# Kernel tuning notes

Hardware: AMD Instinct MI355X
Metric: run time of the kernel (lower is better)

## Reference

```python
import jax, jax.numpy as jnp
import numpy as np

B, S, D, H = 4, 2048, 1024, 16
HD = D // H


def setup_inputs() -> dict:
    key = jax.random.key(0)
    ks = jax.random.split(key, 10)
    x = jax.random.normal(ks[0], (B, S, D), dtype=jnp.float32)
    mask = jnp.zeros((B, 1, 1, S), dtype=jnp.float32)  # 1 = masked, 0 = keep
    sc = 1.0 / np.sqrt(D)
    wq = jax.random.normal(ks[1], (D, D), dtype=jnp.float32) * sc
    wk = jax.random.normal(ks[2], (D, D), dtype=jnp.float32) * sc
    wv = jax.random.normal(ks[3], (D, D), dtype=jnp.float32) * sc
    wo = jax.random.normal(ks[4], (D, D), dtype=jnp.float32) * sc
    bq = jnp.zeros((D,), jnp.float32)
    bk = jnp.zeros((D,), jnp.float32)
    bv = jnp.zeros((D,), jnp.float32)
    bo = jnp.zeros((D,), jnp.float32)
    return {"x": x, "mask": mask, "wq": wq, "bq": bq, "wk": wk, "bk": bk,
            "wv": wv, "bv": bv, "wo": wo, "bo": bo}


def _split_heads(t):
    # (B, S, D) -> (B, H, S, HD)
    return t.reshape(B, -1, H, HD).transpose(0, 2, 1, 3)


def reference(x, mask, wq, bq, wk, bk, wv, bv, wo, bo):
    q = _split_heads(x @ wq + bq)
    k = _split_heads(x @ wk + bk)
    v = _split_heads(x @ wv + bv)
    # scaled dot-product attention (TF tutorial convention: mask*-1e9 added)
    scores = jnp.einsum("bhqd,bhkd->bhqk", q, k) / jnp.sqrt(jnp.float32(HD))
    scores = scores + mask * -1e9
    attn_weights = jax.nn.softmax(scores, axis=-1)  # (B, H, Sq, Sk)
    attn = jnp.einsum("bhqk,bhkd->bhqd", attn_weights, v)
    attn = attn.transpose(0, 2, 1, 3).reshape(B, -1, D)
    out = attn @ wo + bo
    return out, attn_weights
```

## Files before the change

### kernel.cpp

```cpp
#include <hip/hip_runtime.h>
#include <hip/hip_bf16.h>

#define S_LEN  2048
#define DMODEL 1024
#define NHEAD  16
#define HDIM   64
#define BSZ    4

#define C_SCORE  0.18033688f
#define C_MASK  -1.4426950e9f

typedef __bf16 bf16_t;
typedef __bf16 bf16x8 __attribute__((ext_vector_type(8)));
typedef __bf16 bf16x4 __attribute__((ext_vector_type(4)));
typedef float  f32x4  __attribute__((ext_vector_type(4)));

typedef __attribute__((address_space(1))) void as1_void;
typedef __attribute__((address_space(3))) void as3_void;

__device__ __forceinline__ f32x4 mfma16(bf16x8 a, bf16x8 b, f32x4 c) {
    return __builtin_amdgcn_mfma_f32_16x16x32_bf16(a, b, c, 0, 0, 0);
}

__global__ __launch_bounds__(256) void cvt_all(const float* __restrict__ x,
                                               bf16_t* __restrict__ xb,
                                               const float* __restrict__ w0,
                                               const float* __restrict__ w1,
                                               const float* __restrict__ w2,
                                               const float* __restrict__ w3,
                                               bf16_t* __restrict__ wT) {
    __shared__ bf16_t t[64][65];
    const int bid = blockIdx.x;
    if (bid < 4096) {
        const int i0 = bid * 256 + threadIdx.x;
        #pragma unroll
        for (int rep = 0; rep < 2; ++rep) {
            const int i = i0 + rep * 1048576;
            float4 v = ((const float4*)x)[i];
            bf16x4 tv = { (bf16_t)v.x, (bf16_t)v.y, (bf16_t)v.z, (bf16_t)v.w };
            ((bf16x4*)xb)[i] = tv;
        }
        return;
    }
    const int wb = bid - 4096;
    const int wsel = wb >> 8;
    const float* w = wsel == 0 ? w0 : (wsel == 1 ? w1 : (wsel == 2 ? w2 : w3));
    bf16_t* wTo = wT + (size_t)wsel * DMODEL * DMODEL;
    const int rb = wb & 255;
    const int bx = (rb & 15) * 64, by = (rb >> 4) * 64;
    const int tx = threadIdx.x & 63, ty = threadIdx.x >> 6;
    #pragma unroll
    for (int rr = 0; rr < 64; rr += 4)
        t[tx][rr + ty] = (bf16_t)w[(size_t)(bx + rr + ty) * DMODEL + by + tx];
    __syncthreads();
    #pragma unroll
    for (int rr = 0; rr < 64; rr += 4)
        wTo[(size_t)(by + rr + ty) * DMODEL + bx + tx] = t[rr + ty][tx];
}

template <int MODE>
__global__ __launch_bounds__(256) void gemm_bt(const bf16_t* __restrict__ A,
                                               const bf16_t* __restrict__ Bt,
                                               const float* __restrict__ b0,
                                               const float* __restrict__ b1,
                                               const float* __restrict__ b2,
                                               bf16_t* __restrict__ o0,
                                               bf16_t* __restrict__ o1,
                                               bf16_t* __restrict__ o2,
                                               float* __restrict__ of) {
    constexpr int GK = 1024;
    __shared__ __attribute__((aligned(16))) bf16_t smem_ab[8704];
    bf16_t* As = smem_ab;
    bf16_t* Bs = smem_ab + 4096;

    const int tid  = threadIdx.x;
    const int wave = tid >> 6, lane = tid & 63;
    const int col16 = lane & 15, g = lane >> 4;
    const int wr = wave >> 1, wc = wave & 1;
    const int bn0 = blockIdx.x * 128, bm0 = blockIdx.y * 128;

    const int r4 = tid >> 2;
    const int c8 = (tid & 3) * 8;

    f32x4 acc[4][4] = {};

    for (int k0 = 0; k0 < GK; k0 += 32) {
        __syncthreads();
        #pragma unroll
        for (int i = 0; i < 2; ++i) {
            __builtin_amdgcn_global_load_lds(
                (const as1_void*)(A + (size_t)(bm0 + i * 64 + r4) * GK + k0 + c8),
                (as3_void*)(As + (i * 64 + wave * 16) * 32), 16, 0, 0);
            __builtin_amdgcn_global_load_lds(
                (const as1_void*)(Bt + (size_t)(bn0 + i * 64 + r4) * GK + k0 + c8),
                (as3_void*)(Bs + (i * 64 + wave * 16) * 32), 16, 0, 0);
        }
        __syncthreads();

        bf16x8 af[4], bfr[4];
        #pragma unroll
        for (int i = 0; i < 4; ++i) {
            af[i]  = *(const bf16x8*)(As + (wr * 64 + i * 16 + col16) * 32 + g * 8);
            bfr[i] = *(const bf16x8*)(Bs + (wc * 64 + i * 16 + col16) * 32 + g * 8);
        }
        #pragma unroll
        for (int mi = 0; mi < 4; ++mi)
            #pragma unroll
            for (int ni = 0; ni < 4; ++ni)
                acc[mi][ni] = mfma16(af[mi], bfr[ni], acc[mi][ni]);
    }

    if (MODE == 0 && (bn0 >> 10) == 2) {
        const int n1base = bn0 - 2048;
        const int brow = bm0 >> 11;
        const int s0 = bm0 & 2047;
        __syncthreads();
        #pragma unroll
        for (int p = 0; p < 2; ++p) {
            if (p) __syncthreads();
            if (wc == p) {
                #pragma unroll
                for (int ni = 0; ni < 4; ++ni) {
                    const float bv = b2[n1base + p * 64 + ni * 16 + col16];
                    #pragma unroll
                    for (int mi = 0; mi < 4; ++mi) {
                        bf16x4 pv;
                        #pragma unroll
                        for (int r = 0; r < 4; ++r) pv[r] = (bf16_t)(acc[mi][ni][r] + bv);
                        *(bf16x4*)&smem_ab[(ni * 16 + col16) * 136 + wr * 64 + mi * 16 + g * 4] = pv;
                    }
                }
            }
            __syncthreads();
            const int h2 = (n1base + p * 64) >> 6;
            bf16_t* vout = o2 + (((size_t)brow * NHEAD + h2) * HDIM) * S_LEN + s0;
            #pragma unroll
            for (int j = 0; j < 4; ++j) {
                const int unit = j * 256 + tid;
                const int row = unit >> 4;
                const int cu = (unit & 15) * 8;
                bf16x8 v = *(const bf16x8*)&smem_ab[row * 136 + cu];
                *(bf16x8*)(vout + (size_t)row * S_LEN + cu) = v;
            }
        }
        return;
    }

    #pragma unroll
    for (int ni = 0; ni < 4; ++ni) {
        const int gn = bn0 + wc * 64 + ni * 16 + col16;
        if (MODE == 0) {
            const int proj = bn0 >> 10;
            const float* bias = proj == 0 ? b0 : b1;
            bf16_t* outp      = proj == 0 ? o0 : o1;
            const int n1 = gn & 1023, h = n1 >> 6, hd = n1 & 63;
            const float bv = bias[n1];
            #pragma unroll
            for (int mi = 0; mi < 4; ++mi)
                #pragma unroll
                for (int r = 0; r < 4; ++r) {
                    const int gm = bm0 + wr * 64 + mi * 16 + g * 4 + r;
                    const int b = gm >> 11, s = gm & 2047;
                    outp[(((size_t)b * NHEAD + h) * S_LEN + s) * HDIM + hd] =
                        (bf16_t)(acc[mi][ni][r] + bv);
                }
        } else {
            const float bv = b0[gn];
            #pragma unroll
            for (int mi = 0; mi < 4; ++mi)
                #pragma unroll
                for (int r = 0; r < 4; ++r) {
                    const int gm = bm0 + wr * 64 + mi * 16 + g * 4 + r;
                    of[(size_t)gm * DMODEL + gn] = acc[mi][ni][r] + bv;
                }
        }
    }
}

__global__ __launch_bounds__(256, 2) void attn_fused(const bf16_t* __restrict__ Q,
                                                     const bf16_t* __restrict__ K,
                                                     const bf16_t* __restrict__ Vt,
                                                     const float* __restrict__ mask,
                                                     float* __restrict__ attnW,
                                                     bf16_t* __restrict__ ctx) {
    __shared__ __attribute__((aligned(16))) char smem[73728];
    bf16_t (*KsA)[128][64] = (bf16_t(*)[128][64])smem;
    bf16_t (*Ks)[64][64]   = (bf16_t(*)[64][64])smem;
    bf16_t (*Vs)[64][64]   = (bf16_t(*)[64][64])(smem + 16384);
    float  (*Pl)[32][64]   = (float(*)[32][64])(smem + 32768);
    float*  Ml             = (float*)(smem + 65536);

    const int tid = threadIdx.x, wave = tid >> 6, lane = tid & 63;
    const int col16 = lane & 15, g = lane >> 4;
    const int r7 = col16 & 7;

    const int lin = blockIdx.x;
    const int logical = (lin & 7) * 64 + (lin >> 3);
    const int bh = logical >> 3, pp = logical & 7;
    const int b = bh >> 4, h = bh & 15;
    const int qA = pp * 256 + wave * 32;
    const int qB = pp * 256 + 128 + wave * 32;

    const bf16_t* Qb = Q + (size_t)bh * S_LEN * HDIM;
    const bf16_t* Kb = K + (size_t)bh * S_LEN * HDIM;
    const bf16_t* Vb = Vt + (size_t)bh * HDIM * S_LEN;
    const float* mp = mask + (size_t)b * S_LEN;

    #pragma unroll
    for (int i = 0; i < 2; ++i) {
        const int idx = i * 256 + tid;
        f32x4 v = ((const f32x4*)mp)[idx];
        #pragma unroll
        for (int r = 0; r < 4; ++r) v[r] *= C_MASK;
        *(f32x4*)(&Ml[idx * 4]) = v;
    }

    const int srow  = lane >> 3;
    const int sunit = (lane & 7) ^ srow;

    auto stageA = [&](int buf, int it) {
        const int kk0 = it << 7;
        #pragma unroll
        for (int i2 = 0; i2 < 4; ++i2) {
            const int i = wave * 4 + i2;
            __builtin_amdgcn_global_load_lds(
                (const as1_void*)(Kb + (size_t)(kk0 + i * 8 + srow) * HDIM + sunit * 8),
                (as3_void*)(&KsA[buf][i * 8][0]), 16, 0, 0);
        }
    };
    auto stageK = [&](int buf, int it) {
        const int kk0 = it << 6;
        #pragma unroll
        for (int i2 = 0; i2 < 2; ++i2) {
            const int i = wave * 2 + i2;
            __builtin_amdgcn_global_load_lds(
                (const as1_void*)(Kb + (size_t)(kk0 + i * 8 + srow) * HDIM + sunit * 8),
                (as3_void*)(&Ks[buf][i * 8][0]), 16, 0, 0);
        }
    };
    auto stageV = [&](int buf, int it) {
        const int kk0 = it << 6;
        #pragma unroll
        for (int i2 = 0; i2 < 2; ++i2) {
            const int i = wave * 2 + i2;
            __builtin_amdgcn_global_load_lds(
                (const as1_void*)(Vb + (size_t)(i * 8 + srow) * S_LEN + kk0 + sunit * 8),
                (as3_void*)(&Vs[buf][i * 8][0]), 16, 0, 0);
        }
    };
    auto kfrag = [&](int buf, int nj, int kh) {
        return *(const bf16x8*)(&Ks[buf][nj * 16 + col16][(((kh * 4 + g) ^ r7) * 8)]);
    };
    auto vfrag = [&](int buf, int nd, int kh) {
        return *(const bf16x8*)(&Vs[buf][nd * 16 + col16][(((kh * 4 + g) ^ r7) * 8)]);
    };

    bf16x8 qa0[2][2], qa1[2][2];
    #pragma unroll
    for (int hh = 0; hh < 2; ++hh)
        #pragma unroll
        for (int kh = 0; kh < 2; ++kh) {
            qa0[hh][kh] = *(const bf16x8*)(Qb + (size_t)(qA + hh * 16 + col16) * HDIM +
                                           kh * 32 + g * 8);
            qa1[hh][kh] = *(const bf16x8*)(Qb + (size_t)(qB + hh * 16 + col16) * HDIM +
                                           kh * 32 + g * 8);
        }

    f32x4 lacc[2] = {};
    stageA(0, 0);
    __syncthreads();

    for (int it = 0; it < 16; ++it) {
        const int kk0 = it << 7, cur = it & 1;
        if (it < 15) stageA(cur ^ 1, it + 1);
        #pragma unroll
        for (int nj = 0; nj < 8; ++nj) {
            const f32x4 mvr = *(const f32x4*)(&Ml[kk0 + nj * 16 + g * 4]);
            const bf16x8 kf0 = *(const bf16x8*)(&KsA[cur][nj * 16 + col16][((g ^ r7) * 8)]);
            const bf16x8 kf1 = *(const bf16x8*)(&KsA[cur][nj * 16 + col16][(((4 + g) ^ r7) * 8)]);
            f32x4 t0 = {0.f, 0.f, 0.f, 0.f}, t1 = {0.f, 0.f, 0.f, 0.f};
            t0 = mfma16(kf0, qa0[0][0], t0);
            t0 = mfma16(kf1, qa0[0][1], t0);
            t1 = mfma16(kf0, qa0[1][0], t1);
            t1 = mfma16(kf1, qa0[1][1], t1);
            #pragma unroll
            for (int r = 0; r < 4; ++r) {
                lacc[0][r] += exp2f(fmaf(t0[r], C_SCORE, mvr[r]));
                lacc[1][r] += exp2f(fmaf(t1[r], C_SCORE, mvr[r]));
            }
        }
        asm volatile("s_waitcnt vmcnt(0)" ::: "memory");
        __builtin_amdgcn_sched_barrier(0);
        __builtin_amdgcn_s_barrier();
    }

    float crow0[2];
    #pragma unroll
    for (int hh = 0; hh < 2; ++hh) {
        float lr = (lacc[hh][0] + lacc[hh][1]) + (lacc[hh][2] + lacc[hh][3]);
        lr += __shfl_xor(lr, 16);
        lr += __shfl_xor(lr, 32);
        crow0[hh] = -__log2f(lr);
        lacc[hh] = (f32x4){0.f, 0.f, 0.f, 0.f};
    }

    f32x4 o[2][4] = {};
    float* awbase = attnW + ((size_t)bh * S_LEN + qA) * S_LEN;

    stageK(0, 0);
    stageV(0, 0);
    asm volatile("s_waitcnt vmcnt(0)" ::: "memory");
    __builtin_amdgcn_sched_barrier(0);
    __builtin_amdgcn_s_barrier();

    for (int it = 0; it < 32; ++it) {
        const int kk0 = it << 6, cur = it & 1;
        if (it < 31) { stageK(cur ^ 1, it + 1); stageV(cur ^ 1, it + 1); }
        f32x4 mvr[4];
        #pragma unroll
        for (int nj = 0; nj < 4; ++nj)
            mvr[nj] = *(const f32x4*)(&Ml[kk0 + nj * 16 + g * 4]);

        #pragma unroll
        for (int nj = 0; nj < 4; ++nj) {
            const bf16x8 kf0 = kfrag(cur, nj, 0);
            const bf16x8 kf1 = kfrag(cur, nj, 1);
            f32x4 s0 = {0.f, 0.f, 0.f, 0.f}, s1 = {0.f, 0.f, 0.f, 0.f};
            f32x4 u0 = {0.f, 0.f, 0.f, 0.f}, u1 = {0.f, 0.f, 0.f, 0.f};
            s0 = mfma16(kf0, qa0[0][0], s0);
            s0 = mfma16(kf1, qa0[0][1], s0);
            s1 = mfma16(kf0, qa0[1][0], s1);
            s1 = mfma16(kf1, qa0[1][1], s1);
            u0 = mfma16(kf0, qa1[0][0], u0);
            u0 = mfma16(kf1, qa1[0][1], u0);
            u1 = mfma16(kf0, qa1[1][0], u1);
            u1 = mfma16(kf1, qa1[1][1], u1);
            f32x4 pn0, pn1;
            #pragma unroll
            for (int r = 0; r < 4; ++r) {
                const float mm = mvr[nj][r];
                pn0[r] = exp2f(fmaf(s0[r], C_SCORE, mm + crow0[0]));
                pn1[r] = exp2f(fmaf(s1[r], C_SCORE, mm + crow0[1]));
                lacc[0][r] += exp2f(fmaf(u0[r], C_SCORE, mm));
                lacc[1][r] += exp2f(fmaf(u1[r], C_SCORE, mm));
            }
            const int pw = ((nj * 4 + g) ^ r7) * 4;
            *(f32x4*)(&Pl[wave][col16][pw])      = pn0;
            *(f32x4*)(&Pl[wave][16 + col16][pw]) = pn1;
        }

        #pragma unroll
        for (int j = 0; j < 8; ++j) {
            const int row = j * 4 + (lane >> 4);
            const int u = lane & 15;
            const f32x4 v = *(const f32x4*)(&Pl[wave][row][((u ^ (row & 7)) * 4)]);
            __builtin_nontemporal_store(v, (f32x4*)(awbase + (size_t)row * S_LEN + kk0 + u * 4));
        }

        #pragma unroll
        for (int hh = 0; hh < 2; ++hh)
            #pragma unroll
            for (int kh = 0; kh < 2; ++kh) {
                const int u0i = kh * 8 + g * 2;
                const f32x4 a0 = *(const f32x4*)(&Pl[wave][hh * 16 + col16][((u0i ^ r7) * 4)]);
                const f32x4 a1 = *(const f32x4*)(&Pl[wave][hh * 16 + col16][(((u0i + 1) ^ r7) * 4)]);
                bf16x8 pa;
                #pragma unroll
                for (int j = 0; j < 4; ++j) {
                    pa[j]     = (bf16_t)a0[j];
                    pa[4 + j] = (bf16_t)a1[j];
                }
                #pragma unroll
                for (int nd = 0; nd < 4; ++nd)
                    o[hh][nd] = mfma16(vfrag(cur, nd, kh), pa, o[hh][nd]);
            }

        asm volatile("s_waitcnt vmcnt(8)" ::: "memory");
        __builtin_amdgcn_sched_barrier(0);
        __builtin_amdgcn_s_barrier();
    }

    float crow1[2];
    #pragma unroll
    for (int hh = 0; hh < 2; ++hh) {
        float lr = (lacc[hh][0] + lacc[hh][1]) + (lacc[hh][2] + lacc[hh][3]);
        lr += __shfl_xor(lr, 16);
        lr += __shfl_xor(lr, 32);
        crow1[hh] = -__log2f(lr);
    }

    #pragma unroll
    for (int hh = 0; hh < 2; ++hh) {
        bf16_t* cp = ctx + ((size_t)b * S_LEN + qA + hh * 16 + col16) * DMODEL + h * HDIM;
        #pragma unroll
        for (int nd = 0; nd < 4; ++nd) {
            bf16x4 cv;
            #pragma unroll
            for (int r = 0; r < 4; ++r) cv[r] = (bf16_t)o[hh][nd][r];
            *(bf16x4*)(cp + nd * 16 + g * 4) = cv;
        }
        o[hh][0] = o[hh][1] = o[hh][2] = o[hh][3] = (f32x4){0.f, 0.f, 0.f, 0.f};
    }

    awbase = attnW + ((size_t)bh * S_LEN + qB) * S_LEN;

    stageK(0, 0);
    stageV(0, 0);
    asm volatile("s_waitcnt vmcnt(0)" ::: "memory");
    __builtin_amdgcn_sched_barrier(0);
    __builtin_amdgcn_s_barrier();

    for (int it = 0; it < 32; ++it) {
        const int kk0 = it << 6, cur = it & 1;
        if (it < 31) { stageK(cur ^ 1, it + 1); stageV(cur ^ 1, it + 1); }
        f32x4 mvr[4];
        #pragma unroll
        for (int nj = 0; nj < 4; ++nj)
            mvr[nj] = *(const f32x4*)(&Ml[kk0 + nj * 16 + g * 4]);

        #pragma unroll
        for (int nj = 0; nj < 4; ++nj) {
            const bf16x8 kf0 = kfrag(cur, nj, 0);
            const bf16x8 kf1 = kfrag(cur, nj, 1);
            f32x4 t0 = {0.f, 0.f, 0.f, 0.f}, t1 = {0.f, 0.f, 0.f, 0.f};
            t0 = mfma16(kf0, qa1[0][0], t0);
            t0 = mfma16(kf1, qa1[0][1], t0);
            t1 = mfma16(kf0, qa1[1][0], t1);
            t1 = mfma16(kf1, qa1[1][1], t1);
            f32x4 pn0, pn1;
            #pragma unroll
            for (int r = 0; r < 4; ++r) {
                const float mm = mvr[nj][r];
                pn0[r] = exp2f(fmaf(t0[r], C_SCORE, mm + crow1[0]));
                pn1[r] = exp2f(fmaf(t1[r], C_SCORE, mm + crow1[1]));
            }
            const int pw = ((nj * 4 + g) ^ r7) * 4;
            *(f32x4*)(&Pl[wave][col16][pw])      = pn0;
            *(f32x4*)(&Pl[wave][16 + col16][pw]) = pn1;
        }

        #pragma unroll
        for (int j = 0; j < 8; ++j) {
            const int row = j * 4 + (lane >> 4);
            const int u = lane & 15;
            const f32x4 v = *(const f32x4*)(&Pl[wave][row][((u ^ (row & 7)) * 4)]);
            __builtin_nontemporal_store(v, (f32x4*)(awbase + (size_t)row * S_LEN + kk0 + u * 4));
        }

        #pragma unroll
        for (int hh = 0; hh < 2; ++hh)
            #pragma unroll
            for (int kh = 0; kh < 2; ++kh) {
                const int u0i = kh * 8 + g * 2;
                const f32x4 a0 = *(const f32x4*)(&Pl[wave][hh * 16 + col16][((u0i ^ r7) * 4)]);
                const f32x4 a1 = *(const f32x4*)(&Pl[wave][hh * 16 + col16][(((u0i + 1) ^ r7) * 4)]);
                bf16x8 pa;
                #pragma unroll
                for (int j = 0; j < 4; ++j) {
                    pa[j]     = (bf16_t)a0[j];
                    pa[4 + j] = (bf16_t)a1[j];
                }
                #pragma unroll
                for (int nd = 0; nd < 4; ++nd)
                    o[hh][nd] = mfma16(vfrag(cur, nd, kh), pa, o[hh][nd]);
            }

        asm volatile("s_waitcnt vmcnt(8)" ::: "memory");
        __builtin_amdgcn_sched_barrier(0);
        __builtin_amdgcn_s_barrier();
    }

    #pragma unroll
    for (int hh = 0; hh < 2; ++hh) {
        bf16_t* cp = ctx + ((size_t)b * S_LEN + qB + hh * 16 + col16) * DMODEL + h * HDIM;
        #pragma unroll
        for (int nd = 0; nd < 4; ++nd) {
            bf16x4 cv;
            #pragma unroll
            for (int r = 0; r < 4; ++r) cv[r] = (bf16_t)o[hh][nd][r];
            *(bf16x4*)(cp + nd * 16 + g * 4) = cv;
        }
    }
}

extern "C" void kernel_launch(void* const* d_in, const int* in_sizes, int n_in,
                              void* d_out, int out_size, void* d_ws, size_t ws_size,
                              hipStream_t stream) {
    const float* x    = (const float*)d_in[0];
    const float* mask = (const float*)d_in[1];
    const float* wq   = (const float*)d_in[2];
    const float* bq   = (const float*)d_in[3];
    const float* wk   = (const float*)d_in[4];
    const float* bk   = (const float*)d_in[5];
    const float* wv   = (const float*)d_in[6];
    const float* bv   = (const float*)d_in[7];
    const float* wo   = (const float*)d_in[8];
    const float* bo   = (const float*)d_in[9];

    const size_t nX = (size_t)BSZ * S_LEN * DMODEL;
    const size_t nW = (size_t)DMODEL * DMODEL;

    char* ws = (char*)d_ws;
    size_t off = 0;
    bf16_t* xb     = (bf16_t*)(ws + off); off += nX * 2;
    bf16_t* wqkvT  = (bf16_t*)(ws + off); off += 3 * nW * 2;
    bf16_t* woT    = (bf16_t*)(ws + off); off += nW * 2;
    bf16_t* qbh    = (bf16_t*)(ws + off); off += nX * 2;
    bf16_t* kbh    = (bf16_t*)(ws + off); off += nX * 2;
    bf16_t* vtb    = (bf16_t*)(ws + off); off += nX * 2;
    bf16_t* ctx    = (bf16_t*)(ws + off); off += nX * 2;
    if (ws_size < off) return;

    float* outp  = (float*)d_out;
    float* attnW = outp + nX;

    cvt_all<<<5120, 256, 0, stream>>>(x, xb, wq, wk, wv, wo, wqkvT);

    gemm_bt<0><<<dim3(24, 64), 256, 0, stream>>>(xb, wqkvT, bq, bk, bv,
                                                 qbh, kbh, vtb, nullptr);

    attn_fused<<<512, 256, 0, stream>>>(qbh, kbh, vtb, mask, attnW, ctx);

    gemm_bt<2><<<dim3(8, 64), 256, 0, stream>>>(ctx, woT, bo, nullptr, nullptr,
                                                nullptr, nullptr, nullptr, outp);
}
```

Measured before the change: 375.9 us.

## Compute both query-block row sums upfront and merge the two output passes

```diff
diff --git a/kernel.cpp b/kernel.cpp
--- a/kernel.cpp
+++ b/kernel.cpp
@@ -266,7 +266,7 @@
                                            kh * 32 + g * 8);
         }
 
-    f32x4 lacc[2] = {};
+    f32x4 lacc0[2] = {}, lacc1[2] = {};
     stageA(0, 0);
     __syncthreads();
 
@@ -279,14 +279,21 @@
             const bf16x8 kf0 = *(const bf16x8*)(&KsA[cur][nj * 16 + col16][((g ^ r7) * 8)]);
             const bf16x8 kf1 = *(const bf16x8*)(&KsA[cur][nj * 16 + col16][(((4 + g) ^ r7) * 8)]);
             f32x4 t0 = {0.f, 0.f, 0.f, 0.f}, t1 = {0.f, 0.f, 0.f, 0.f};
+            f32x4 u0 = {0.f, 0.f, 0.f, 0.f}, u1 = {0.f, 0.f, 0.f, 0.f};
             t0 = mfma16(kf0, qa0[0][0], t0);
             t0 = mfma16(kf1, qa0[0][1], t0);
             t1 = mfma16(kf0, qa0[1][0], t1);
             t1 = mfma16(kf1, qa0[1][1], t1);
+            u0 = mfma16(kf0, qa1[0][0], u0);
+            u0 = mfma16(kf1, qa1[0][1], u0);
+            u1 = mfma16(kf0, qa1[1][0], u1);
+            u1 = mfma16(kf1, qa1[1][1], u1);
             #pragma unroll
             for (int r = 0; r < 4; ++r) {
-                lacc[0][r] += exp2f(fmaf(t0[r], C_SCORE, mvr[r]));
-                lacc[1][r] += exp2f(fmaf(t1[r], C_SCORE, mvr[r]));
+                lacc0[0][r] += exp2f(fmaf(t0[r], C_SCORE, mvr[r]));
+                lacc0[1][r] += exp2f(fmaf(t1[r], C_SCORE, mvr[r]));
+                lacc1[0][r] += exp2f(fmaf(u0[r], C_SCORE, mvr[r]));
+                lacc1[1][r] += exp2f(fmaf(u1[r], C_SCORE, mvr[r]));
             }
         }
         asm volatile("s_waitcnt vmcnt(0)" ::: "memory");
@@ -294,18 +301,22 @@
         __builtin_amdgcn_s_barrier();
     }
 
-    float crow0[2];
+    float crow0[2], crow1[2];
     #pragma unroll
     for (int hh = 0; hh < 2; ++hh) {
-        float lr = (lacc[hh][0] + lacc[hh][1]) + (lacc[hh][2] + lacc[hh][3]);
-        lr += __shfl_xor(lr, 16);
-        lr += __shfl_xor(lr, 32);
-        crow0[hh] = -__log2f(lr);
-        lacc[hh] = (f32x4){0.f, 0.f, 0.f, 0.f};
-    }
-
-    f32x4 o[2][4] = {};
-    float* awbase = attnW + ((size_t)bh * S_LEN + qA) * S_LEN;
+        float lr0 = (lacc0[hh][0] + lacc0[hh][1]) + (lacc0[hh][2] + lacc0[hh][3]);
+        lr0 += __shfl_xor(lr0, 16);
+        lr0 += __shfl_xor(lr0, 32);
+        crow0[hh] = -__log2f(lr0);
+        float lr1 = (lacc1[hh][0] + lacc1[hh][1]) + (lacc1[hh][2] + lacc1[hh][3]);
+        lr1 += __shfl_xor(lr1, 16);
+        lr1 += __shfl_xor(lr1, 32);
+        crow1[hh] = -__log2f(lr1);
+    }
+
+    f32x4 o0[2][4] = {}, o1[2][4] = {};
+    float* awA = attnW + ((size_t)bh * S_LEN + qA) * S_LEN;
+    float* awB = attnW + ((size_t)bh * S_LEN + qB) * S_LEN;
 
     stageK(0, 0);
     stageV(0, 0);
@@ -316,6 +327,7 @@
     for (int it = 0; it < 32; ++it) {
         const int kk0 = it << 6, cur = it & 1;
         if (it < 31) { stageK(cur ^ 1, it + 1); stageV(cur ^ 1, it + 1); }
+        __builtin_amdgcn_sched_barrier(0);
         f32x4 mvr[4];
         #pragma unroll
         for (int nj = 0; nj < 4; ++nj)
@@ -326,37 +338,28 @@
             const bf16x8 kf0 = kfrag(cur, nj, 0);
             const bf16x8 kf1 = kfrag(cur, nj, 1);
             f32x4 s0 = {0.f, 0.f, 0.f, 0.f}, s1 = {0.f, 0.f, 0.f, 0.f};
-            f32x4 u0 = {0.f, 0.f, 0.f, 0.f}, u1 = {0.f, 0.f, 0.f, 0.f};
             s0 = mfma16(kf0, qa0[0][0], s0);
             s0 = mfma16(kf1, qa0[0][1], s0);
             s1 = mfma16(kf0, qa0[1][0], s1);
             s1 = mfma16(kf1, qa0[1][1], s1);
-            u0 = mfma16(kf0, qa1[0][0], u0);
-            u0 = mfma16(kf1, qa1[0][1], u0);
-            u1 = mfma16(kf0, qa1[1][0], u1);
-            u1 = mfma16(kf1, qa1[1][1], u1);
             f32x4 pn0, pn1;
             #pragma unroll
             for (int r = 0; r < 4; ++r) {
                 const float mm = mvr[nj][r];
                 pn0[r] = exp2f(fmaf(s0[r], C_SCORE, mm + crow0[0]));
                 pn1[r] = exp2f(fmaf(s1[r], C_SCORE, mm + crow0[1]));
-                lacc[0][r] += exp2f(fmaf(u0[r], C_SCORE, mm));
-                lacc[1][r] += exp2f(fmaf(u1[r], C_SCORE, mm));
             }
             const int pw = ((nj * 4 + g) ^ r7) * 4;
             *(f32x4*)(&Pl[wave][col16][pw])      = pn0;
             *(f32x4*)(&Pl[wave][16 + col16][pw]) = pn1;
         }
-
         #pragma unroll
         for (int j = 0; j < 8; ++j) {
             const int row = j * 4 + (lane >> 4);
             const int u = lane & 15;
             const f32x4 v = *(const f32x4*)(&Pl[wave][row][((u ^ (row & 7)) * 4)]);
-            __builtin_nontemporal_store(v, (f32x4*)(awbase + (size_t)row * S_LEN + kk0 + u * 4));
-        }
-
+            __builtin_nontemporal_store(v, (f32x4*)(awA + (size_t)row * S_LEN + kk0 + u * 4));
+        }
         #pragma unroll
         for (int hh = 0; hh < 2; ++hh)
             #pragma unroll
@@ -372,81 +375,36 @@
                 }
                 #pragma unroll
                 for (int nd = 0; nd < 4; ++nd)
-                    o[hh][nd] = mfma16(vfrag(cur, nd, kh), pa, o[hh][nd]);
-            }
-
-        asm volatile("s_waitcnt vmcnt(8)" ::: "memory");
-        __builtin_amdgcn_sched_barrier(0);
-        __builtin_amdgcn_s_barrier();
-    }
-
-    float crow1[2];
-    #pragma unroll
-    for (int hh = 0; hh < 2; ++hh) {
-        float lr = (lacc[hh][0] + lacc[hh][1]) + (lacc[hh][2] + lacc[hh][3]);
-        lr += __shfl_xor(lr, 16);
-        lr += __shfl_xor(lr, 32);
-        crow1[hh] = -__log2f(lr);
-    }
-
-    #pragma unroll
-    for (int hh = 0; hh < 2; ++hh) {
-        bf16_t* cp = ctx + ((size_t)b * S_LEN + qA + hh * 16 + col16) * DMODEL + h * HDIM;
-        #pragma unroll
-        for (int nd = 0; nd < 4; ++nd) {
-            bf16x4 cv;
-            #pragma unroll
-            for (int r = 0; r < 4; ++r) cv[r] = (bf16_t)o[hh][nd][r];
-            *(bf16x4*)(cp + nd * 16 + g * 4) = cv;
-        }
-        o[hh][0] = o[hh][1] = o[hh][2] = o[hh][3] = (f32x4){0.f, 0.f, 0.f, 0.f};
-    }
-
-    awbase = attnW + ((size_t)bh * S_LEN + qB) * S_LEN;
-
-    stageK(0, 0);
-    stageV(0, 0);
-    asm volatile("s_waitcnt vmcnt(0)" ::: "memory");
-    __builtin_amdgcn_sched_barrier(0);
-    __builtin_amdgcn_s_barrier();
-
-    for (int it = 0; it < 32; ++it) {
-        const int kk0 = it << 6, cur = it & 1;
-        if (it < 31) { stageK(cur ^ 1, it + 1); stageV(cur ^ 1, it + 1); }
-        f32x4 mvr[4];
-        #pragma unroll
-        for (int nj = 0; nj < 4; ++nj)
-            mvr[nj] = *(const f32x4*)(&Ml[kk0 + nj * 16 + g * 4]);
+                    o0[hh][nd] = mfma16(vfrag(cur, nd, kh), pa, o0[hh][nd]);
+            }
 
         #pragma unroll
         for (int nj = 0; nj < 4; ++nj) {
             const bf16x8 kf0 = kfrag(cur, nj, 0);
             const bf16x8 kf1 = kfrag(cur, nj, 1);
-            f32x4 t0 = {0.f, 0.f, 0.f, 0.f}, t1 = {0.f, 0.f, 0.f, 0.f};
-            t0 = mfma16(kf0, qa1[0][0], t0);
-            t0 = mfma16(kf1, qa1[0][1], t0);
-            t1 = mfma16(kf0, qa1[1][0], t1);
-            t1 = mfma16(kf1, qa1[1][1], t1);
+            f32x4 s0 = {0.f, 0.f, 0.f, 0.f}, s1 = {0.f, 0.f, 0.f, 0.f};
+            s0 = mfma16(kf0, qa1[0][0], s0);
+            s0 = mfma16(kf1, qa1[0][1], s0);
+            s1 = mfma16(kf0, qa1[1][0], s1);
+            s1 = mfma16(kf1, qa1[1][1], s1);
             f32x4 pn0, pn1;
             #pragma unroll
             for (int r = 0; r < 4; ++r) {
                 const float mm = mvr[nj][r];
-                pn0[r] = exp2f(fmaf(t0[r], C_SCORE, mm + crow1[0]));
-                pn1[r] = exp2f(fmaf(t1[r], C_SCORE, mm + crow1[1]));
+                pn0[r] = exp2f(fmaf(s0[r], C_SCORE, mm + crow1[0]));
+                pn1[r] = exp2f(fmaf(s1[r], C_SCORE, mm + crow1[1]));
             }
             const int pw = ((nj * 4 + g) ^ r7) * 4;
             *(f32x4*)(&Pl[wave][col16][pw])      = pn0;
             *(f32x4*)(&Pl[wave][16 + col16][pw]) = pn1;
         }
-
         #pragma unroll
         for (int j = 0; j < 8; ++j) {
             const int row = j * 4 + (lane >> 4);
             const int u = lane & 15;
             const f32x4 v = *(const f32x4*)(&Pl[wave][row][((u ^ (row & 7)) * 4)]);
-            __builtin_nontemporal_store(v, (f32x4*)(awbase + (size_t)row * S_LEN + kk0 + u * 4));
-        }
-
+            __builtin_nontemporal_store(v, (f32x4*)(awB + (size_t)row * S_LEN + kk0 + u * 4));
+        }
         #pragma unroll
         for (int hh = 0; hh < 2; ++hh)
             #pragma unroll
@@ -462,23 +420,28 @@
                 }
                 #pragma unroll
                 for (int nd = 0; nd < 4; ++nd)
-                    o[hh][nd] = mfma16(vfrag(cur, nd, kh), pa, o[hh][nd]);
-            }
-
-        asm volatile("s_waitcnt vmcnt(8)" ::: "memory");
+                    o1[hh][nd] = mfma16(vfrag(cur, nd, kh), pa, o1[hh][nd]);
+            }
+
+        asm volatile("s_waitcnt vmcnt(16)" ::: "memory");
         __builtin_amdgcn_sched_barrier(0);
         __builtin_amdgcn_s_barrier();
     }
 
     #pragma unroll
     for (int hh = 0; hh < 2; ++hh) {
-        bf16_t* cp = ctx + ((size_t)b * S_LEN + qB + hh * 16 + col16) * DMODEL + h * HDIM;
+        bf16_t* cpA = ctx + ((size_t)b * S_LEN + qA + hh * 16 + col16) * DMODEL + h * HDIM;
+        bf16_t* cpB = ctx + ((size_t)b * S_LEN + qB + hh * 16 + col16) * DMODEL + h * HDIM;
         #pragma unroll
         for (int nd = 0; nd < 4; ++nd) {
-            bf16x4 cv;
-            #pragma unroll
-            for (int r = 0; r < 4; ++r) cv[r] = (bf16_t)o[hh][nd][r];
-            *(bf16x4*)(cp + nd * 16 + g * 4) = cv;
+            bf16x4 cv0, cv1;
+            #pragma unroll
+            for (int r = 0; r < 4; ++r) {
+                cv0[r] = (bf16_t)o0[hh][nd][r];
+                cv1[r] = (bf16_t)o1[hh][nd][r];
+            }
+            *(bf16x4*)(cpA + nd * 16 + g * 4) = cv0;
+            *(bf16x4*)(cpB + nd * 16 + g * 4) = cv1;
         }
     }
 }
```

New measurement: 379.2 us. About the same (+0.9%).
